# Kernel optimization log

Hardware: AMD Instinct MI355X
Metric: run time of the kernel (lower is better)

## Reference

```python
import jax, jax.numpy as jnp
import numpy as np

# LeNet-5 C3 connectivity table: mask[h, j] == 1 iff input map h feeds output map j.
MASK = np.array([
    [1,0,0,0,1,1,1,0,0,1,1,1,1,0,1,1],
    [1,1,0,0,0,1,1,1,0,0,1,1,1,1,0,1],
    [1,1,1,0,0,0,1,1,1,0,0,1,0,1,1,1],
    [0,1,1,1,0,0,1,1,1,1,0,0,1,0,1,1],
    [0,0,1,1,1,0,0,1,1,1,1,0,1,1,0,1],
    [0,0,0,1,1,1,0,0,1,1,1,1,0,1,1,1],
], dtype=bool)
IDX = [jnp.asarray(np.where(MASK[h])[0]) for h in range(6)]  # 10 outputs per input ch

B, CIN, COUT, K = 65536, 6, 16, 5


def setup_inputs() -> dict:
    key = jax.random.key(0)
    kx, kw, kb = jax.random.split(key, 3)
    x = jax.random.normal(kx, (B, CIN, 14, 14), dtype=jnp.float32)
    weights = jax.random.normal(kw, (CIN, 10, K, K), dtype=jnp.float32) * 0.1
    bias = jax.random.normal(kb, (1, COUT, 1, 1), dtype=jnp.float32) * 0.1
    return {"x": x, "weights": weights, "bias": bias}


def reference(x, weights, bias):
    # out spatial: 14 - 5 + 1 = 10 (VALID conv, stride 1, no bias in per-channel convs)
    out = jnp.zeros((x.shape[0], COUT, 10, 10), dtype=x.dtype)
    for h in range(CIN):  # small fixed structural loop over 6 input channels
        y = jax.lax.conv_general_dilated(
            x[:, h:h + 1],                 # [B, 1, 14, 14]
            weights[h][:, None],           # [10, 1, 5, 5]
            window_strides=(1, 1),
            padding="VALID",
            dimension_numbers=("NCHW", "OIHW", "NCHW"),
        )                                   # [B, 10, 10, 10]
        out = out.at[:, IDX[h]].set(y)
    return out + bias
```

## Files before the change

### kernel.cpp

```cpp
#include <hip/hip_runtime.h>


#define NB 8
#define THREADS 256
#define XPITCH 788

__device__ __constant__ int C3_HREL[16] = {0,1,2,3,3,3,1,2,3,3,3,3,2,3,3,3};
__device__ __constant__ int C3_WIDX[16] = {20,30,40,50,51,52,33,43,53,54,55,56,47,57,58,59};

__global__ __launch_bounds__(THREADS, 2)
void c3_kernel(const float* __restrict__ x,
               const float* __restrict__ w,
               const float* __restrict__ bias,
               float* __restrict__ out) {
    __shared__ float sx[NB * XPITCH];
    __shared__ float so[NB * 1600];

    const int t = threadIdx.x;

    {
        const float4* __restrict__ x4 = (const float4*)x;
        const long long base = (long long)blockIdx.x * NB;
#pragma unroll
        for (int i = 0; i < (NB * 196 + THREADS - 1) / THREADS; ++i) {
            int idx = t + i * THREADS;
            if (idx < NB * 196) {
                int bat = idx / 196;
                int q   = idx - bat * 196;
                float4 v = x4[(base + bat) * 294 + 98 + q];
                *(float4*)&sx[bat * XPITCH + q * 4] = v;
            }
        }
    }

    const int half = t & 1;
    const int j    = (t >> 1) & 15;
    const int bloc = t >> 5;

    const int   hrel = C3_HREL[j];
    const float bj   = bias[j];

    const float* __restrict__ wp = w + C3_WIDX[j] * 25;
    float wr[25];
#pragma unroll
    for (int i = 0; i < 25; ++i) wr[i] = wp[i];

    __syncthreads();

    const float* __restrict__ xp = &sx[bloc * XPITCH + hrel * 196];
    const int r0 = half * 5;

    float xw[5][14];
#pragma unroll
    for (int r = 0; r < 4; ++r) {
        const float2* rp = (const float2*)(xp + (r0 + r) * 14);
#pragma unroll
        for (int i = 0; i < 7; ++i) {
            float2 v = rp[i];
            xw[r][2 * i] = v.x;
            xw[r][2 * i + 1] = v.y;
        }
    }

    float* sbase = &so[bloc * 1600 + j * 100 + r0 * 10];

#pragma unroll
    for (int orow = 0; orow < 5; ++orow) {
        {
            const float2* rp = (const float2*)(xp + (r0 + orow + 4) * 14);
            float* d = xw[(orow + 4) % 5];
#pragma unroll
            for (int i = 0; i < 7; ++i) {
                float2 v = rp[i];
                d[2 * i] = v.x;
                d[2 * i + 1] = v.y;
            }
        }

        float acc[10];
#pragma unroll
        for (int c = 0; c < 10; ++c) acc[c] = bj;

#pragma unroll
        for (int u = 0; u < 5; ++u) {
            const float* row = xw[(orow + u) % 5];
#pragma unroll
            for (int v = 0; v < 5; ++v) {
                const float wv = wr[u * 5 + v];
#pragma unroll
                for (int c = 0; c < 10; ++c)
                    acc[c] = fmaf(wv, row[c + v], acc[c]);
            }
        }

        float2* sp = (float2*)(sbase + orow * 10);
#pragma unroll
        for (int i = 0; i < 5; ++i) sp[i] = make_float2(acc[2 * i], acc[2 * i + 1]);
    }

    __syncthreads();

    const float4* __restrict__ src = (const float4*)so;
    float4* __restrict__ dst = (float4*)(out + (size_t)blockIdx.x * (NB * 1600));
    constexpr int NQ = NB * 1600 / 4;
#pragma unroll
    for (int i = 0; i < (NQ + THREADS - 1) / THREADS; ++i) {
        int idx = t + i * THREADS;
        if (idx < NQ) dst[idx] = src[idx];
    }
}

extern "C" void kernel_launch(void* const* d_in, const int* in_sizes, int n_in,
                              void* d_out, int out_size, void* d_ws, size_t ws_size,
                              hipStream_t stream) {
    const float* x    = (const float*)d_in[0];
    const float* w    = (const float*)d_in[1];
    const float* bias = (const float*)d_in[2];
    float* out        = (float*)d_out;

    const int B = in_sizes[0] / (6 * 14 * 14);
    const int nblocks = B / NB;

    hipLaunchKernelGGL(c3_kernel, dim3(nblocks), dim3(THREADS), 0, stream,
                       x, w, bias, out);
}
```

Baseline: 616.7 us.

## Write outputs directly to global memory, one thread per full output map

Drops the shared-memory output staging buffer and the second barrier. Each thread now computes all 10 rows of one output map and writes row pairs straight to global memory as float4 stores. The block shrinks to 128 threads with a higher occupancy hint, which cuts LDS use and may raise the number of resident blocks. The cost is that global stores now stride by 100 floats across lanes instead of being fully coalesced, and each thread does twice as much sequential work.

```diff
diff --git a/kernel.cpp b/kernel.cpp
--- a/kernel.cpp
+++ b/kernel.cpp
@@ -2,19 +2,18 @@
 
 
 #define NB 8
-#define THREADS 256
-#define XPITCH 788
+#define THREADS 128
+#define XPITCH 792
 
 __device__ __constant__ int C3_HREL[16] = {0,1,2,3,3,3,1,2,3,3,3,3,2,3,3,3};
 __device__ __constant__ int C3_WIDX[16] = {20,30,40,50,51,52,33,43,53,54,55,56,47,57,58,59};
 
-__global__ __launch_bounds__(THREADS, 2)
+__global__ __launch_bounds__(THREADS, 3)
 void c3_kernel(const float* __restrict__ x,
                const float* __restrict__ w,
                const float* __restrict__ bias,
                float* __restrict__ out) {
     __shared__ float sx[NB * XPITCH];
-    __shared__ float so[NB * 1600];
 
     const int t = threadIdx.x;
 
@@ -33,9 +32,8 @@
         }
     }
 
-    const int half = t & 1;
-    const int j    = (t >> 1) & 15;
-    const int bloc = t >> 5;
+    const int j    = t & 15;
+    const int bloc = t >> 4;
 
     const int   hrel = C3_HREL[j];
     const float bj   = bias[j];
@@ -48,31 +46,31 @@
     __syncthreads();
 
     const float* __restrict__ xp = &sx[bloc * XPITCH + hrel * 196];
-    const int r0 = half * 5;
 
     float xw[5][14];
 #pragma unroll
     for (int r = 0; r < 4; ++r) {
-        const float2* rp = (const float2*)(xp + (r0 + r) * 14);
+        const float2* rp = (const float2*)(xp + r * 14);
 #pragma unroll
         for (int i = 0; i < 7; ++i) {
             float2 v = rp[i];
-            xw[r][2 * i] = v.x;
+            xw[r][2 * i]     = v.x;
             xw[r][2 * i + 1] = v.y;
         }
     }
 
-    float* sbase = &so[bloc * 1600 + j * 100 + r0 * 10];
+    float* __restrict__ outp = out + ((size_t)blockIdx.x * NB + bloc) * 1600 + j * 100;
+    float prev[10];
 
 #pragma unroll
-    for (int orow = 0; orow < 5; ++orow) {
+    for (int orow = 0; orow < 10; ++orow) {
         {
-            const float2* rp = (const float2*)(xp + (r0 + orow + 4) * 14);
+            const float2* rp = (const float2*)(xp + (orow + 4) * 14);
             float* d = xw[(orow + 4) % 5];
 #pragma unroll
             for (int i = 0; i < 7; ++i) {
                 float2 v = rp[i];
-                d[2 * i] = v.x;
+                d[2 * i]     = v.x;
                 d[2 * i + 1] = v.y;
             }
         }
@@ -93,20 +91,17 @@
             }
         }
 
-        float2* sp = (float2*)(sbase + orow * 10);
+        if (orow & 1) {
+            float4* __restrict__ dst = (float4*)(outp + (orow - 1) * 10);
+            dst[0] = make_float4(prev[0], prev[1], prev[2], prev[3]);
+            dst[1] = make_float4(prev[4], prev[5], prev[6], prev[7]);
+            dst[2] = make_float4(prev[8], prev[9], acc[0], acc[1]);
+            dst[3] = make_float4(acc[2],  acc[3],  acc[4],  acc[5]);
+            dst[4] = make_float4(acc[6],  acc[7],  acc[8],  acc[9]);
+        } else {
 #pragma unroll
-        for (int i = 0; i < 5; ++i) sp[i] = make_float2(acc[2 * i], acc[2 * i + 1]);
-    }
-
-    __syncthreads();
-
-    const float4* __restrict__ src = (const float4*)so;
-    float4* __restrict__ dst = (float4*)(out + (size_t)blockIdx.x * (NB * 1600));
-    constexpr int NQ = NB * 1600 / 4;
-#pragma unroll
-    for (int i = 0; i < (NQ + THREADS - 1) / THREADS; ++i) {
-        int idx = t + i * THREADS;
-        if (idx < NQ) dst[idx] = src[idx];
+            for (int c = 0; c < 10; ++c) prev[c] = acc[c];
+        }
     }
 }
 
```

Result: slower. 709.7 us (+15.1%).
